# Kernel optimization log

Hardware: AMD Instinct MI355X
Metric: run time of the kernel (lower is better)

Reference implementation:

```python
import jax, jax.numpy as jnp
import numpy as np

NEG_INF = -1e15  # matches masked_fill value -1000000000000000.0
ALPHA = 0.2      # leakyReLU negative slope


def setup_inputs() -> dict:
    key = jax.random.key(0)
    k1, k2, k3, k4 = jax.random.split(key, 4)
    N, F_IN, F_OUT = 8192, 256, 64
    x = jax.random.normal(k1, (N, F_IN), dtype=jnp.float32)
    mask = jax.random.randint(k2, (N, N), 0, 2, dtype=jnp.int32)
    trans = jax.random.normal(k3, (F_IN, F_OUT), dtype=jnp.float32) * 0.1
    attn = jax.random.normal(k4, (2 * F_OUT, 1), dtype=jnp.float32) * 0.1
    return {"x": x, "mask": mask, "trans": trans, "attn": attn}


def reference(x, mask, trans, attn):
    d = trans.shape[1]
    h = x @ trans                                  # [N, d]
    e1 = h @ attn[:d, :]                           # [N, 1]
    e2 = h @ attn[d:, :]                           # [N, 1]
    scores = jax.nn.leaky_relu(e1 + e2.T, negative_slope=ALPHA)  # [N, N]
    masked = jnp.where(mask == 0, NEG_INF, scores)
    attention = jax.nn.softmax(masked, axis=1)
    return attention @ h                           # [N, d]
```

## Files before the change

### kernel.cpp

```cpp
#include <hip/hip_runtime.h>
#include <hip/hip_bf16.h>
#include <math.h>

#define N 8192
#define FIN 256
#define D 64
#define ALPHA 0.2f
#define SROW 1040
#define WBUF (16 * SROW)
#define CS 2048

typedef __attribute__((ext_vector_type(8))) short bf16x8;
typedef __attribute__((ext_vector_type(4))) float f32x4;

__global__ __launch_bounds__(256) void k_h_e(
    const float* __restrict__ x, const float* __restrict__ trans,
    const float* __restrict__ attn,
    __hip_bfloat16* __restrict__ hF, float* __restrict__ e1, float* __restrict__ e2)
{
    __shared__ float xs[8 * FIN];
    __shared__ __hip_bfloat16 hl[8 * D];
    const int t = threadIdx.x;
    const int r0 = blockIdx.x * 8;

    #pragma unroll
    for (int v = 0; v < 2; ++v) {
        int idx = t + 256 * v;
        ((float4*)xs)[idx] = ((const float4*)(x + (size_t)r0 * FIN))[idx];
    }
    __syncthreads();

    const int lane = t & 63, w = t >> 6;
    const float* xa = xs + (2 * w) * FIN;
    const float* xb = xs + (2 * w + 1) * FIN;
    float acca = 0.f, accb = 0.f;
    #pragma unroll 8
    for (int k = 0; k < FIN; ++k) {
        const float tv = trans[k * D + lane];
        acca = fmaf(xa[k], tv, acca);
        accb = fmaf(xb[k], tv, accb);
    }
    const int ra = r0 + 2 * w, rb = ra + 1;

    const float a1 = attn[lane], a2 = attn[D + lane];
    float p1a = acca * a1, p2a = acca * a2;
    float p1b = accb * a1, p2b = accb * a2;
    #pragma unroll
    for (int mm = 1; mm <= 32; mm <<= 1) {
        p1a += __shfl_xor(p1a, mm);
        p2a += __shfl_xor(p2a, mm);
        p1b += __shfl_xor(p1b, mm);
        p2b += __shfl_xor(p2b, mm);
    }
    if (lane == 0) { e1[ra] = p1a; e2[ra] = p2a; e1[rb] = p1b; e2[rb] = p2b; }

    hl[(2 * w) * D + lane]     = __float2bfloat16(acca);
    hl[(2 * w + 1) * D + lane] = __float2bfloat16(accb);
    __syncthreads();
    if (t < D) {
        const int q = t >> 4, m = t & 15;
        const int cb = r0 >> 5, jgrp = (r0 >> 3) & 3;
        union { bf16x8 v; __hip_bfloat16 h[8]; } o;
        #pragma unroll
        for (int r = 0; r < 8; ++r) o.h[r] = hl[r * D + q * 16 + m];
        *(bf16x8*)(hF + (((size_t)cb * 4 + q) * 64 + jgrp * 16 + m) * 8) = o.v;
    }
}

__global__ __launch_bounds__(256) void k_attn(
    const int* __restrict__ mask, const __hip_bfloat16* __restrict__ hF,
    const float* __restrict__ e1, const float* __restrict__ e2,
    float* __restrict__ out)
{
    __shared__ __align__(16) char smem[4 * WBUF];
    __shared__ float lw[4][16];
    const int t = threadIdx.x;
    const int lane = t & 63, wave = t >> 6;
    const int i0 = blockIdx.x * 16;
    const int c0 = wave * CS;
    const int m = lane & 15, quad = lane >> 4;
    const int row = i0 + m;
    const float er = e1[row];

    char* sw = smem + wave * WBUF;
    const char* swm = sw + m * SROW;
    const __hip_bfloat16* hfp = hF + (((size_t)(c0 >> 5)) * 4 * 64 + lane) * 8;

    f32x4 acc0 = {0.f, 0.f, 0.f, 0.f};
    f32x4 acc1 = {0.f, 0.f, 0.f, 0.f};
    f32x4 acc2 = {0.f, 0.f, 0.f, 0.f};
    f32x4 acc3 = {0.f, 0.f, 0.f, 0.f};
    float lsum = 0.f;

    const int nss = CS >> 8;

    for (int ss = 0; ss < nss; ++ss) {
        const int cb0 = c0 + ss * 256;
        #pragma unroll
        for (int r = 0; r < 16; ++r) {
            const int* g = mask + (size_t)(i0 + r) * N + cb0 + lane * 4;
            char* l = sw + r * SROW + lane * 16;
            __builtin_amdgcn_global_load_lds(
                (const __attribute__((address_space(1))) void*)g,
                (__attribute__((address_space(3))) void*)l, 16, 0, 2 );
        }
        __builtin_amdgcn_s_waitcnt(0x0F70);

        const int itg0 = ss * 8;
        bf16x8 pb0, pb1, pb2, pb3; float4 pea, peb;
        {
            const size_t ito = (size_t)itg0 * 2048;
            pb0 = *(const bf16x8*)(hfp + ito);
            pb1 = *(const bf16x8*)(hfp + ito + 512);
            pb2 = *(const bf16x8*)(hfp + ito + 1024);
            pb3 = *(const bf16x8*)(hfp + ito + 1536);
            const int jb = cb0 + quad * 8;
            pea = *(const float4*)(e2 + jb);
            peb = *(const float4*)(e2 + jb + 4);
        }
        #pragma unroll
        for (int p = 0; p < 8; ++p) {
            const bf16x8 b0 = pb0, b1 = pb1, b2 = pb2, b3 = pb3;
            const float4 ea = pea, eb = peb;
            if (p < 7) {
                const size_t ito = (size_t)(itg0 + p + 1) * 2048;
                pb0 = *(const bf16x8*)(hfp + ito);
                pb1 = *(const bf16x8*)(hfp + ito + 512);
                pb2 = *(const bf16x8*)(hfp + ito + 1024);
                pb3 = *(const bf16x8*)(hfp + ito + 1536);
                const int jb = cb0 + (p + 1) * 32 + quad * 8;
                pea = *(const float4*)(e2 + jb);
                peb = *(const float4*)(e2 + jb + 4);
            }
            const int4 m0 = *(const int4*)(swm + p * 128 + quad * 32);
            const int4 m1 = *(const int4*)(swm + p * 128 + quad * 32 + 16);

            float s0 = er + ea.x; s0 = s0 > 0.f ? s0 : ALPHA * s0;
            float s1 = er + ea.y; s1 = s1 > 0.f ? s1 : ALPHA * s1;
            float s2 = er + ea.z; s2 = s2 > 0.f ? s2 : ALPHA * s2;
            float s3 = er + ea.w; s3 = s3 > 0.f ? s3 : ALPHA * s3;
            float s4 = er + eb.x; s4 = s4 > 0.f ? s4 : ALPHA * s4;
            float s5 = er + eb.y; s5 = s5 > 0.f ? s5 : ALPHA * s5;
            float s6 = er + eb.z; s6 = s6 > 0.f ? s6 : ALPHA * s6;
            float s7 = er + eb.w; s7 = s7 > 0.f ? s7 : ALPHA * s7;
            const float p0 = m0.x ? __expf(s0) : 0.f;
            const float p1 = m0.y ? __expf(s1) : 0.f;
            const float p2 = m0.z ? __expf(s2) : 0.f;
            const float p3 = m0.w ? __expf(s3) : 0.f;
            const float p4 = m1.x ? __expf(s4) : 0.f;
            const float p5 = m1.y ? __expf(s5) : 0.f;
            const float p6 = m1.z ? __expf(s6) : 0.f;
            const float p7 = m1.w ? __expf(s7) : 0.f;

            union { bf16x8 v; __hip_bfloat162 h2[4]; } af;
            af.h2[0] = __float22bfloat162_rn(make_float2(p0, p1));
            af.h2[1] = __float22bfloat162_rn(make_float2(p2, p3));
            af.h2[2] = __float22bfloat162_rn(make_float2(p4, p5));
            af.h2[3] = __float22bfloat162_rn(make_float2(p6, p7));

            lsum += ((p0 + p1) + (p2 + p3)) + ((p4 + p5) + (p6 + p7));

            acc0 = __builtin_amdgcn_mfma_f32_16x16x32_bf16(af.v, b0, acc0, 0, 0, 0);
            acc1 = __builtin_amdgcn_mfma_f32_16x16x32_bf16(af.v, b1, acc1, 0, 0, 0);
            acc2 = __builtin_amdgcn_mfma_f32_16x16x32_bf16(af.v, b2, acc2, 0, 0, 0);
            acc3 = __builtin_amdgcn_mfma_f32_16x16x32_bf16(af.v, b3, acc3, 0, 0, 0);
        }
    }

    lsum += __shfl_xor(lsum, 16);
    lsum += __shfl_xor(lsum, 32);
    if (quad == 0) lw[wave][m] = lsum;

    __syncthreads();
    float* cw = (float*)smem;
    #pragma unroll
    for (int reg = 0; reg < 4; ++reg) {
        float* rbase = cw + (wave * 16 + quad * 4 + reg) * 64;
        rbase[m     ] = acc0[reg];
        rbase[m + 16] = acc1[reg];
        rbase[m + 32] = acc2[reg];
        rbase[m + 48] = acc3[reg];
    }
    __syncthreads();
    #pragma unroll
    for (int rr = 0; rr < 4; ++rr) {
        const int idx = rr * 256 + t;
        const int r = idx >> 6, c = idx & 63;
        float s = ((cw[(0 * 16 + r) * 64 + c] + cw[(1 * 16 + r) * 64 + c])
                +   cw[(2 * 16 + r) * 64 + c]) + cw[(3 * 16 + r) * 64 + c];
        float l = ((lw[0][r] + lw[1][r]) + lw[2][r]) + lw[3][r];
        out[(size_t)(i0 + r) * D + c] = s / l;
    }
}

extern "C" void kernel_launch(void* const* d_in, const int* in_sizes, int n_in,
                              void* d_out, int out_size, void* d_ws, size_t ws_size,
                              hipStream_t stream) {
    const float* x     = (const float*)d_in[0];
    const int*   mask  = (const int*)d_in[1];
    const float* trans = (const float*)d_in[2];
    const float* attn  = (const float*)d_in[3];
    float* out = (float*)d_out;

    char* ws = (char*)d_ws;
    __hip_bfloat16* hF = (__hip_bfloat16*)ws;
    char* p = ws + (size_t)D * N * sizeof(__hip_bfloat16);
    float* e1 = (float*)p;            p += (size_t)N * sizeof(float);
    float* e2 = (float*)p;            p += (size_t)N * sizeof(float);

    k_h_e<<<N / 8, 256, 0, stream>>>(x, trans, attn, hF, e1, e2);
    k_attn<<<N / 16, 256, 0, stream>>>(mask, hF, e1, e2, out);
}
```

Baseline: 382.8 us.

## Load mask directly into registers with nontemporal prefetch instead of LDS staging

The attention kernel stops staging 16-row mask tiles into shared memory with global_load_lds and a full waitcnt. Each lane now loads its own mask row segment straight into registers with nontemporal loads, prefetched four iterations ahead in a rotating register set. This removes the per-256-column stall and frees most of the LDS, and launch bounds request three blocks per SM for more occupancy. The cost is more register pressure and less coalesced mask reads, since each lane reads 32 bytes per row instead of whole contiguous rows.

```diff
diff --git a/kernel.cpp b/kernel.cpp
--- a/kernel.cpp
+++ b/kernel.cpp
@@ -6,12 +6,11 @@
 #define FIN 256
 #define D 64
 #define ALPHA 0.2f
-#define SROW 1040
-#define WBUF (16 * SROW)
 #define CS 2048
 
 typedef __attribute__((ext_vector_type(8))) short bf16x8;
 typedef __attribute__((ext_vector_type(4))) float f32x4;
+typedef __attribute__((ext_vector_type(4))) int i32x4;
 
 __global__ __launch_bounds__(256) void k_h_e(
     const float* __restrict__ x, const float* __restrict__ trans,
@@ -67,12 +66,12 @@
     }
 }
 
-__global__ __launch_bounds__(256) void k_attn(
+__global__ __launch_bounds__(256, 3) void k_attn(
     const int* __restrict__ mask, const __hip_bfloat16* __restrict__ hF,
     const float* __restrict__ e1, const float* __restrict__ e2,
     float* __restrict__ out)
 {
-    __shared__ __align__(16) char smem[4 * WBUF];
+    __shared__ float cw[4 * 16 * 64];
     __shared__ float lw[4][16];
     const int t = threadIdx.x;
     const int lane = t & 63, wave = t >> 6;
@@ -82,9 +81,9 @@
     const int row = i0 + m;
     const float er = e1[row];
 
-    char* sw = smem + wave * WBUF;
-    const char* swm = sw + m * SROW;
     const __hip_bfloat16* hfp = hF + (((size_t)(c0 >> 5)) * 4 * 64 + lane) * 8;
+    const i32x4* mp = (const i32x4*)(mask + (size_t)row * N + c0 + quad * 8);
+    const float* ep = e2 + c0 + quad * 8;
 
     f32x4 acc0 = {0.f, 0.f, 0.f, 0.f};
     f32x4 acc1 = {0.f, 0.f, 0.f, 0.f};
@@ -92,87 +91,82 @@
     f32x4 acc3 = {0.f, 0.f, 0.f, 0.f};
     float lsum = 0.f;
 
-    const int nss = CS >> 8;
-
-    for (int ss = 0; ss < nss; ++ss) {
-        const int cb0 = c0 + ss * 256;
-        #pragma unroll
-        for (int r = 0; r < 16; ++r) {
-            const int* g = mask + (size_t)(i0 + r) * N + cb0 + lane * 4;
-            char* l = sw + r * SROW + lane * 16;
-            __builtin_amdgcn_global_load_lds(
-                (const __attribute__((address_space(1))) void*)g,
-                (__attribute__((address_space(3))) void*)l, 16, 0, 2 );
-        }
-        __builtin_amdgcn_s_waitcnt(0x0F70);
-
-        const int itg0 = ss * 8;
-        bf16x8 pb0, pb1, pb2, pb3; float4 pea, peb;
-        {
-            const size_t ito = (size_t)itg0 * 2048;
-            pb0 = *(const bf16x8*)(hfp + ito);
-            pb1 = *(const bf16x8*)(hfp + ito + 512);
-            pb2 = *(const bf16x8*)(hfp + ito + 1024);
-            pb3 = *(const bf16x8*)(hfp + ito + 1536);
-            const int jb = cb0 + quad * 8;
-            pea = *(const float4*)(e2 + jb);
-            peb = *(const float4*)(e2 + jb + 4);
-        }
-        #pragma unroll
-        for (int p = 0; p < 8; ++p) {
-            const bf16x8 b0 = pb0, b1 = pb1, b2 = pb2, b3 = pb3;
-            const float4 ea = pea, eb = peb;
-            if (p < 7) {
-                const size_t ito = (size_t)(itg0 + p + 1) * 2048;
-                pb0 = *(const bf16x8*)(hfp + ito);
-                pb1 = *(const bf16x8*)(hfp + ito + 512);
-                pb2 = *(const bf16x8*)(hfp + ito + 1024);
-                pb3 = *(const bf16x8*)(hfp + ito + 1536);
-                const int jb = cb0 + (p + 1) * 32 + quad * 8;
-                pea = *(const float4*)(e2 + jb);
-                peb = *(const float4*)(e2 + jb + 4);
-            }
-            const int4 m0 = *(const int4*)(swm + p * 128 + quad * 32);
-            const int4 m1 = *(const int4*)(swm + p * 128 + quad * 32 + 16);
-
-            float s0 = er + ea.x; s0 = s0 > 0.f ? s0 : ALPHA * s0;
-            float s1 = er + ea.y; s1 = s1 > 0.f ? s1 : ALPHA * s1;
-            float s2 = er + ea.z; s2 = s2 > 0.f ? s2 : ALPHA * s2;
-            float s3 = er + ea.w; s3 = s3 > 0.f ? s3 : ALPHA * s3;
-            float s4 = er + eb.x; s4 = s4 > 0.f ? s4 : ALPHA * s4;
-            float s5 = er + eb.y; s5 = s5 > 0.f ? s5 : ALPHA * s5;
-            float s6 = er + eb.z; s6 = s6 > 0.f ? s6 : ALPHA * s6;
-            float s7 = er + eb.w; s7 = s7 > 0.f ? s7 : ALPHA * s7;
-            const float p0 = m0.x ? __expf(s0) : 0.f;
-            const float p1 = m0.y ? __expf(s1) : 0.f;
-            const float p2 = m0.z ? __expf(s2) : 0.f;
-            const float p3 = m0.w ? __expf(s3) : 0.f;
-            const float p4 = m1.x ? __expf(s4) : 0.f;
-            const float p5 = m1.y ? __expf(s5) : 0.f;
-            const float p6 = m1.z ? __expf(s6) : 0.f;
-            const float p7 = m1.w ? __expf(s7) : 0.f;
-
-            union { bf16x8 v; __hip_bfloat162 h2[4]; } af;
-            af.h2[0] = __float22bfloat162_rn(make_float2(p0, p1));
-            af.h2[1] = __float22bfloat162_rn(make_float2(p2, p3));
-            af.h2[2] = __float22bfloat162_rn(make_float2(p4, p5));
-            af.h2[3] = __float22bfloat162_rn(make_float2(p6, p7));
-
-            lsum += ((p0 + p1) + (p2 + p3)) + ((p4 + p5) + (p6 + p7));
-
-            acc0 = __builtin_amdgcn_mfma_f32_16x16x32_bf16(af.v, b0, acc0, 0, 0, 0);
-            acc1 = __builtin_amdgcn_mfma_f32_16x16x32_bf16(af.v, b1, acc1, 0, 0, 0);
-            acc2 = __builtin_amdgcn_mfma_f32_16x16x32_bf16(af.v, b2, acc2, 0, 0, 0);
-            acc3 = __builtin_amdgcn_mfma_f32_16x16x32_bf16(af.v, b3, acc3, 0, 0, 0);
-        }
-    }
+    i32x4 pmA0 = __builtin_nontemporal_load(mp + 0);
+    i32x4 pmB0 = __builtin_nontemporal_load(mp + 1);
+    i32x4 pmA1 = __builtin_nontemporal_load(mp + 8);
+    i32x4 pmB1 = __builtin_nontemporal_load(mp + 9);
+    i32x4 pmA2 = __builtin_nontemporal_load(mp + 16);
+    i32x4 pmB2 = __builtin_nontemporal_load(mp + 17);
+    i32x4 pmA3 = __builtin_nontemporal_load(mp + 24);
+    i32x4 pmB3 = __builtin_nontemporal_load(mp + 25);
+
+    bf16x8 pb0 = *(const bf16x8*)(hfp);
+    bf16x8 pb1 = *(const bf16x8*)(hfp + 512);
+    bf16x8 pb2 = *(const bf16x8*)(hfp + 1024);
+    bf16x8 pb3 = *(const bf16x8*)(hfp + 1536);
+    float4 pea = *(const float4*)(ep);
+    float4 peb = *(const float4*)(ep + 4);
+
+#define ITER(J, IT, LASTC4)                                                    \
+    {                                                                          \
+        const i32x4 m0 = pmA##J, m1 = pmB##J;                                  \
+        if (!(LASTC4)) {                                                       \
+            pmA##J = __builtin_nontemporal_load(mp + ((IT) + 4) * 8);          \
+            pmB##J = __builtin_nontemporal_load(mp + ((IT) + 4) * 8 + 1);      \
+        }                                                                      \
+        const bf16x8 b0 = pb0, b1 = pb1, b2 = pb2, b3 = pb3;                   \
+        const float4 ea = pea, eb = peb;                                       \
+        if ((IT) < 63) {                                                       \
+            const size_t ito = (size_t)((IT) + 1) * 2048;                      \
+            pb0 = *(const bf16x8*)(hfp + ito);                                 \
+            pb1 = *(const bf16x8*)(hfp + ito + 512);                           \
+            pb2 = *(const bf16x8*)(hfp + ito + 1024);                          \
+            pb3 = *(const bf16x8*)(hfp + ito + 1536);                          \
+            pea = *(const float4*)(ep + ((IT) + 1) * 32);                      \
+            peb = *(const float4*)(ep + ((IT) + 1) * 32 + 4);                  \
+        }                                                                      \
+        float s0 = er + ea.x; s0 = s0 > 0.f ? s0 : ALPHA * s0;                 \
+        float s1 = er + ea.y; s1 = s1 > 0.f ? s1 : ALPHA * s1;                 \
+        float s2 = er + ea.z; s2 = s2 > 0.f ? s2 : ALPHA * s2;                 \
+        float s3 = er + ea.w; s3 = s3 > 0.f ? s3 : ALPHA * s3;                 \
+        float s4 = er + eb.x; s4 = s4 > 0.f ? s4 : ALPHA * s4;                 \
+        float s5 = er + eb.y; s5 = s5 > 0.f ? s5 : ALPHA * s5;                 \
+        float s6 = er + eb.z; s6 = s6 > 0.f ? s6 : ALPHA * s6;                 \
+        float s7 = er + eb.w; s7 = s7 > 0.f ? s7 : ALPHA * s7;                 \
+        const float p0 = m0[0] ? __expf(s0) : 0.f;                             \
+        const float p1 = m0[1] ? __expf(s1) : 0.f;                             \
+        const float p2 = m0[2] ? __expf(s2) : 0.f;                             \
+        const float p3 = m0[3] ? __expf(s3) : 0.f;                             \
+        const float p4 = m1[0] ? __expf(s4) : 0.f;                             \
+        const float p5 = m1[1] ? __expf(s5) : 0.f;                             \
+        const float p6 = m1[2] ? __expf(s6) : 0.f;                             \
+        const float p7 = m1[3] ? __expf(s7) : 0.f;                             \
+        union { bf16x8 v; __hip_bfloat162 h2[4]; } af;                         \
+        af.h2[0] = __float22bfloat162_rn(make_float2(p0, p1));                 \
+        af.h2[1] = __float22bfloat162_rn(make_float2(p2, p3));                 \
+        af.h2[2] = __float22bfloat162_rn(make_float2(p4, p5));                 \
+        af.h2[3] = __float22bfloat162_rn(make_float2(p6, p7));                 \
+        lsum += ((p0 + p1) + (p2 + p3)) + ((p4 + p5) + (p6 + p7));             \
+        acc0 = __builtin_amdgcn_mfma_f32_16x16x32_bf16(af.v, b0, acc0, 0, 0, 0); \
+        acc1 = __builtin_amdgcn_mfma_f32_16x16x32_bf16(af.v, b1, acc1, 0, 0, 0); \
+        acc2 = __builtin_amdgcn_mfma_f32_16x16x32_bf16(af.v, b2, acc2, 0, 0, 0); \
+        acc3 = __builtin_amdgcn_mfma_f32_16x16x32_bf16(af.v, b3, acc3, 0, 0, 0); \
+    }
+
+    for (int c4 = 0; c4 < 16; ++c4) {
+        const int base = c4 * 4;
+        const bool lastc4 = (c4 == 15);
+        ITER(0, base + 0, lastc4)
+        ITER(1, base + 1, lastc4)
+        ITER(2, base + 2, lastc4)
+        ITER(3, base + 3, lastc4)
+    }
+#undef ITER
 
     lsum += __shfl_xor(lsum, 16);
     lsum += __shfl_xor(lsum, 32);
     if (quad == 0) lw[wave][m] = lsum;
 
-    __syncthreads();
-    float* cw = (float*)smem;
     #pragma unroll
     for (int reg = 0; reg < 4; ++reg) {
         float* rbase = cw + (wave * 16 + quad * 4 + reg) * 64;
```

Result: slower. 402.1 us (+5.0%).
